# Kernel optimization log

Hardware: AMD Instinct MI355X
Metric: run time of the kernel (lower is better)

Reference implementation:

```python
import jax, jax.numpy as jnp
import numpy as np

SEQ, D, H = 4096, 1024, 1024


def setup_inputs() -> dict:
    key = jax.random.key(0)
    k_x, k_w1, k_b1, k_w2, k_b2 = jax.random.split(key, 5)
    std = 1.0 / np.sqrt(H)
    inputs = jax.random.normal(k_x, (SEQ, D), dtype=jnp.float32)
    W1 = jax.random.uniform(k_w1, (3 * H, 2 * D), minval=-std, maxval=std, dtype=jnp.float32)
    b1 = jax.random.uniform(k_b1, (3 * H,), minval=-std, maxval=std, dtype=jnp.float32)
    W2 = jax.random.uniform(k_w2, (H, H), minval=-std, maxval=std, dtype=jnp.float32)
    b2 = jax.random.uniform(k_b2, (H,), minval=-std, maxval=std, dtype=jnp.float32)
    return {"inputs": inputs, "W1": W1, "b1": b1, "W2": W2, "b2": b2}


def reference(inputs, W1, b1, W2, b2):
    # Exclusive prefix sum along seq: s[t] = sum_{i<t} x[i]
    s = jnp.concatenate(
        [jnp.zeros((1, inputs.shape[1]), dtype=inputs.dtype),
         jnp.cumsum(inputs[:-1], axis=0)], axis=0)
    v = jnp.concatenate([inputs, s], axis=1)            # [S, 2D]
    gates = v @ W1.T + b1                               # [S, 3H]
    ig, fg, h = jnp.split(gates, 3, axis=1)
    ig = jax.nn.sigmoid(ig)
    fg = jax.nn.sigmoid(fg)
    h = jnp.tanh(h) @ W2.T + b2                         # [S, H]
    hr = h * ig
    return (fg, hr)
```

## Files before the change

kernel.cpp:

```cpp
#include <hip/hip_runtime.h>
#include <cmath>

#define S_SEQ 4096
#define HD 1024
#define NG 3072
#define CHR 32
#define NCH 128
#define NZ 4

typedef _Float16 half8_t __attribute__((ext_vector_type(8)));
typedef _Float16 half4_t __attribute__((ext_vector_type(4)));
typedef float f32x4_t __attribute__((ext_vector_type(4)));

__device__ __forceinline__ void gload_lds16(const void* g, void* l) {
  __builtin_amdgcn_global_load_lds(
      (const __attribute__((address_space(1))) void*)g,
      (__attribute__((address_space(3))) void*)l, 16, 0, 0);
}

__device__ __forceinline__ float sigmoidf_(float x) {
  return 1.f / (1.f + __expf(-x));
}
__device__ __forceinline__ float tanhf_(float x) {
  return 1.f - 2.f / (__expf(2.f * x) + 1.f);
}

#define SCAN_BLOCKS 128
#define CONV_BLOCKS 7168
__global__ void prep(const float* __restrict__ W1, const float* __restrict__ W2,
                     _Float16* __restrict__ w1h, _Float16* __restrict__ w2h,
                     const float* __restrict__ x, _Float16* __restrict__ A,
                     _Float16* __restrict__ xsum) {
  const int bid = blockIdx.x;
  if (bid < SCAN_BLOCKS) {
    const int c = bid;
    const int j = threadIdx.x * 4;
    const int t0 = c * CHR;
    float4 run = make_float4(0.f, 0.f, 0.f, 0.f);
    for (int t = t0; t < t0 + CHR; t += 8) {
      float4 v[8];
#pragma unroll
      for (int u = 0; u < 8; ++u)
        v[u] = *(const float4*)&x[(size_t)(t + u) * HD + j];
#pragma unroll
      for (int u = 0; u < 8; ++u) {
        half4_t hx, hs;
        hx[0] = (_Float16)v[u].x;  hx[1] = (_Float16)v[u].y;
        hx[2] = (_Float16)v[u].z;  hx[3] = (_Float16)v[u].w;
        hs[0] = (_Float16)run.x;   hs[1] = (_Float16)run.y;
        hs[2] = (_Float16)run.z;   hs[3] = (_Float16)run.w;
        *(half4_t*)&A[(size_t)(t + u) * 2048 + j] = hx;
        *(half4_t*)&A[(size_t)(t + u) * 2048 + 1024 + j] = hs;
        run.x += v[u].x; run.y += v[u].y; run.z += v[u].z; run.w += v[u].w;
      }
    }
    half4_t hxs;
    hxs[0] = (_Float16)run.x; hxs[1] = (_Float16)run.y;
    hxs[2] = (_Float16)run.z; hxs[3] = (_Float16)run.w;
    *(half4_t*)&xsum[(size_t)c * HD + j] = hxs;
  } else {
    const int n1 = NG * 2048 / 4;
    int i = (bid - SCAN_BLOCKS) * 256 + threadIdx.x;
    const float* src = (i < n1) ? (W1 + (size_t)i * 4)
                                : (W2 + (size_t)(i - n1) * 4);
    _Float16* dst = (i < n1) ? (w1h + (size_t)i * 4)
                             : (w2h + (size_t)(i - n1) * 4);
    float4 v = *(const float4*)src;
    half4_t h;
    h[0] = (_Float16)v.x; h[1] = (_Float16)v.y;
    h[2] = (_Float16)v.z; h[3] = (_Float16)v.w;
    *(half4_t*)dst = h;
  }
}

__global__ void scan_part(const float* __restrict__ praw,
                          const float* __restrict__ b1,
                          float* __restrict__ pout) {
  int j = blockIdx.x * 256 + threadIdx.x;
  const size_t SP = (size_t)NCH * NG;
  float run = b1[j];
  for (int c = 0; c < NCH; c += 8) {
    float v[8];
#pragma unroll
    for (int u = 0; u < 8; ++u) {
      size_t i0 = (size_t)(c + u) * NG + j;
      v[u] = (praw[i0] + praw[i0 + SP]) + (praw[i0 + 2 * SP] + praw[i0 + 3 * SP]);
    }
#pragma unroll
    for (int u = 0; u < 8; ++u) {
      pout[(size_t)(c + u) * NG + j] = run;
      run += v[u];
    }
  }
}

__global__ __launch_bounds__(256, 2)
void gemm_part(const _Float16* __restrict__ A, const _Float16* __restrict__ B,
               float* __restrict__ C) {
  __shared__ _Float16 As[128 * 32];
  __shared__ _Float16 Bs[128 * 32];

  const int tid = threadIdx.x;
  const int lane = tid & 63;
  const int wid = tid >> 6;
  const int wr = wid >> 1;
  const int wc = wid & 1;

  const int n0 = blockIdx.x * 128;
  const int koff = blockIdx.z * (1024 / NZ);

  const int srow = lane >> 2;
  const int scol = (lane & 3) << 3;

  const _Float16* gA = A + (size_t)(wid * 32 + srow) * 1024 + koff + scol;
  const _Float16* gB = B + (size_t)(n0 + wid * 32 + srow) * 2048 + koff + scol;
  _Float16* lA = As + (wid * 32) * 32;
  _Float16* lB = Bs + (wid * 32) * 32;

  f32x4_t acc[4][4] = {};

  const int fr = lane & 15;
  const int fk = (lane >> 4) << 3;

  for (int kk = 0; kk < 1024 / NZ; kk += 32) {
    gload_lds16(gA + kk,                    lA);
    gload_lds16(gA + kk + (size_t)16*1024,  lA + 16 * 32);
    gload_lds16(gB + kk,                    lB);
    gload_lds16(gB + kk + (size_t)16*2048,  lB + 16 * 32);
    __syncthreads();

    half8_t af[4], bf[4];
#pragma unroll
    for (int m = 0; m < 4; ++m)
      af[m] = *(const half8_t*)&As[(wr * 64 + m * 16 + fr) * 32 + fk];
#pragma unroll
    for (int n = 0; n < 4; ++n)
      bf[n] = *(const half8_t*)&Bs[(wc * 64 + n * 16 + fr) * 32 + fk];
#pragma unroll
    for (int m = 0; m < 4; ++m)
#pragma unroll
      for (int n = 0; n < 4; ++n)
        acc[m][n] = __builtin_amdgcn_mfma_f32_16x16x32_f16(af[m], bf[n],
                                                           acc[m][n], 0, 0, 0);
    __syncthreads();
  }

  float* Cz = C + (size_t)blockIdx.z * NCH * NG;
  const int crow = wr * 64 + ((lane >> 4) << 2);
  const int ccol = n0 + wc * 64 + fr;
#pragma unroll
  for (int m = 0; m < 4; ++m)
#pragma unroll
    for (int n = 0; n < 4; ++n) {
      const int col = ccol + n * 16;
#pragma unroll
      for (int r = 0; r < 4; ++r)
        Cz[(size_t)(crow + m * 16 + r) * NG + col] = acc[m][n][r];
    }
}

#define BARX __builtin_amdgcn_s_barrier()
#define PR1 __builtin_amdgcn_s_setprio(1)
#define PR0 __builtin_amdgcn_s_setprio(0)

__global__ __launch_bounds__(256, 2)
void gemm1_k64(const _Float16* __restrict__ A, const _Float16* __restrict__ B,
               const float* __restrict__ part, _Float16* __restrict__ igb,
               float* __restrict__ out0, _Float16* __restrict__ th) {
  constexpr int KS = 2048;
  constexpr int NT = 32;
  __shared__ __align__(16) _Float16 sA[2][128 * 64];
  __shared__ __align__(16) _Float16 sB[2][192 * 64];

  const int tid = threadIdx.x;
  const int l = tid & 63;
  const int wid = tid >> 6;
  const int wr = wid >> 1;
  const int wc = wid & 1;

  const int bid = blockIdx.x;
  const int xcd = bid & 7;
  const int q = bid >> 3;
  const int by = xcd * 4 + q / 16;
  const int bx = q % 16;
  const int m0 = by * 128;
  const int n0 = bx * 192;

  const int rB = tid >> 3;
  const int cB = tid & 7;
  const int csw = (cB ^ (rB & 7)) << 3;
  const _Float16* gA0 = A + (size_t)(m0 + rB) * KS + csw;
  const _Float16* gB0 = B + (size_t)(n0 + rB) * KS + csw;
  const int dsto = rB * 64 + cB * 8;

#define STG(bb, kt) do {                                               \
    const int kk_ = (kt) * 64;                                         \
    _Pragma("unroll")                                                  \
    for (int j = 0; j < 4; ++j)                                        \
      gload_lds16(gA0 + (size_t)(32 * j) * KS + kk_,                   \
                  (_Float16*)&sA[bb][dsto + j * 2048]);                \
    _Pragma("unroll")                                                  \
    for (int j = 0; j < 6; ++j)                                        \
      gload_lds16(gB0 + (size_t)(32 * j) * KS + kk_,                   \
                  (_Float16*)&sB[bb][dsto + j * 2048]);                \
  } while (0)

  const int fr = l & 15;
  const int kq = l >> 4;

#define RDA(dst, M, H, bb) do {                                        \
    const int row_ = wr * 64 + (M) * 16 + fr;                          \
    dst = *(const half8_t*)&sA[bb][row_ * 64 +                         \
          ((((H) * 4 + kq) ^ (row_ & 7)) << 3)];                       \
  } while (0)
#define RDB(dst, N_, H, bb) do {                                       \
    const int row_ = wc * 96 + (N_) * 16 + fr;                         \
    dst = *(const half8_t*)&sB[bb][row_ * 64 +                         \
          ((((H) * 4 + kq) ^ (row_ & 7)) << 3)];                       \
  } while (0)

  f32x4_t acc[4][6] = {};

#define BODY(t, bb) do {                                               \
    const int nt_ = ((t) + 1 < NT) ? (t) + 1 : NT - 1;                 \
    STG((bb) ^ 1, nt_);                                                \
    half8_t af[4][2], bf[6][2];                                        \
    _Pragma("unroll")                                                  \
    for (int m = 0; m < 4; ++m) {                                      \
      RDA(af[m][0], m, 0, bb); RDA(af[m][1], m, 1, bb);                \
    }                                                                  \
    _Pragma("unroll")                                                  \
    for (int n = 0; n < 6; ++n) {                                      \
      RDB(bf[n][0], n, 0, bb); RDB(bf[n][1], n, 1, bb);                \
    }                                                                  \
    PR1;                                                               \
    _Pragma("unroll")                                                  \
    for (int m = 0; m < 4; ++m)                                        \
      _Pragma("unroll")                                                \
      for (int n = 0; n < 6; ++n) {                                    \
        acc[m][n] = __builtin_amdgcn_mfma_f32_16x16x32_f16(            \
            af[m][0], bf[n][0], acc[m][n], 0, 0, 0);                   \
        acc[m][n] = __builtin_amdgcn_mfma_f32_16x16x32_f16(            \
            af[m][1], bf[n][1], acc[m][n], 0, 0, 0);                   \
      }                                                                \
    PR0;                                                               \
    asm volatile("s_waitcnt vmcnt(0)" ::: "memory");                   \
    BARX;                                                              \
  } while (0)

  STG(0, 0);
  asm volatile("s_waitcnt vmcnt(0)" ::: "memory");
  BARX;

#pragma unroll 1
  for (int t2 = 0; t2 < NT / 2; ++t2) {
    BODY(2 * t2,     0);
    BODY(2 * t2 + 1, 1);
  }

  const int crow = m0 + wr * 64 + ((l >> 4) << 2);
  const int ccol = n0 + wc * 96 + fr;

  float pv[2][6];
  const int cbase = crow >> 5;
#pragma unroll
  for (int h = 0; h < 2; ++h)
#pragma unroll
    for (int n = 0; n < 6; ++n)
      pv[h][n] = part[(size_t)(cbase + h) * NG + ccol + n * 16];

#pragma unroll
  for (int m = 0; m < 4; ++m)
#pragma unroll
    for (int n = 0; n < 6; ++n) {
      const int col = ccol + n * 16;
#pragma unroll
      for (int r = 0; r < 4; ++r) {
        const int row = crow + m * 16 + r;
        float g = acc[m][n][r] + pv[m >> 1][n];
        if (col < 1024)
          igb[(size_t)row * HD + col] = (_Float16)sigmoidf_(g);
        else if (col < 2048)
          out0[(size_t)row * HD + (col - 1024)] = sigmoidf_(g);
        else
          th[(size_t)row * HD + (col - 2048)] = (_Float16)tanhf_(g);
      }
    }
#undef STG
#undef RDA
#undef RDB
#undef BODY
}

__global__ __launch_bounds__(256, 2)
void gemm2_k64(const _Float16* __restrict__ A, const _Float16* __restrict__ B,
               float* __restrict__ outf,
               const float* __restrict__ bias, const _Float16* __restrict__ mulh) {
  constexpr int KS = 1024;
  constexpr int NT = 16;
  __shared__ __align__(16) _Float16 sA[2][128 * 64];
  __shared__ __align__(16) _Float16 sB[2][64 * 64];

  const int tid = threadIdx.x;
  const int l = tid & 63;
  const int wid = tid >> 6;
  const int wr = wid >> 1;
  const int wc = wid & 1;

  const int bid = blockIdx.x;
  const int xcd = bid & 7;
  const int q = bid >> 3;
  const int by = xcd * 4 + q / 16;
  const int bx = q % 16;
  const int m0 = by * 128;
  const int n0 = bx * 64;

  const int rB = tid >> 3;
  const int cB = tid & 7;
  const int csw = (cB ^ (rB & 7)) << 3;
  const _Float16* gA0 = A + (size_t)(m0 + rB) * KS + csw;
  const _Float16* gB0 = B + (size_t)(n0 + rB) * KS + csw;
  const int dsto = rB * 64 + cB * 8;

#define STG(bb, kt) do {                                               \
    const int kk_ = (kt) * 64;                                         \
    _Pragma("unroll")                                                  \
    for (int j = 0; j < 4; ++j)                                        \
      gload_lds16(gA0 + (size_t)(32 * j) * KS + kk_,                   \
                  (_Float16*)&sA[bb][dsto + j * 2048]);                \
    _Pragma("unroll")                                                  \
    for (int j = 0; j < 2; ++j)                                        \
      gload_lds16(gB0 + (size_t)(32 * j) * KS + kk_,                   \
                  (_Float16*)&sB[bb][dsto + j * 2048]);                \
  } while (0)

  const int fr = l & 15;
  const int kq = l >> 4;

#define RDA(dst, M, H, bb) do {                                        \
    const int row_ = wr * 64 + (M) * 16 + fr;                          \
    dst = *(const half8_t*)&sA[bb][row_ * 64 +                         \
          ((((H) * 4 + kq) ^ (row_ & 7)) << 3)];                       \
  } while (0)
#define RDB(dst, N_, H, bb) do {                                       \
    const int row_ = wc * 32 + (N_) * 16 + fr;                         \
    dst = *(const half8_t*)&sB[bb][row_ * 64 +                         \
          ((((H) * 4 + kq) ^ (row_ & 7)) << 3)];                       \
  } while (0)

  f32x4_t acc[4][2] = {};

#define BODY(t, bb) do {                                               \
    const int nt_ = ((t) + 1 < NT) ? (t) + 1 : NT - 1;                 \
    STG((bb) ^ 1, nt_);                                                \
    half8_t af[4][2], bf[2][2];                                        \
    _Pragma("unroll")                                                  \
    for (int m = 0; m < 4; ++m) {                                      \
      RDA(af[m][0], m, 0, bb); RDA(af[m][1], m, 1, bb);                \
    }                                                                  \
    _Pragma("unroll")                                                  \
    for (int n = 0; n < 2; ++n) {                                      \
      RDB(bf[n][0], n, 0, bb); RDB(bf[n][1], n, 1, bb);                \
    }                                                                  \
    PR1;                                                               \
    _Pragma("unroll")                                                  \
    for (int m = 0; m < 4; ++m)                                        \
      _Pragma("unroll")                                                \
      for (int n = 0; n < 2; ++n) {                                    \
        acc[m][n] = __builtin_amdgcn_mfma_f32_16x16x32_f16(            \
            af[m][0], bf[n][0], acc[m][n], 0, 0, 0);                   \
        acc[m][n] = __builtin_amdgcn_mfma_f32_16x16x32_f16(            \
            af[m][1], bf[n][1], acc[m][n], 0, 0, 0);                   \
      }                                                                \
    PR0;                                                               \
    asm volatile("s_waitcnt vmcnt(0)" ::: "memory");                   \
    BARX;                                                              \
  } while (0)

  STG(0, 0);
  asm volatile("s_waitcnt vmcnt(0)" ::: "memory");
  BARX;

#pragma unroll 1
  for (int t2 = 0; t2 < NT / 2; ++t2) {
    BODY(2 * t2,     0);
    BODY(2 * t2 + 1, 1);
  }

  const int crow = m0 + wr * 64 + ((l >> 4) << 2);
  const int ccol = n0 + wc * 32 + fr;
#pragma unroll
  for (int m = 0; m < 4; ++m)
#pragma unroll
    for (int n = 0; n < 2; ++n) {
      const int col = ccol + n * 16;
#pragma unroll
      for (int r = 0; r < 4; ++r) {
        const int row = crow + m * 16 + r;
        size_t idx = (size_t)row * HD + col;
        outf[idx] = (acc[m][n][r] + bias[col]) * (float)mulh[idx];
      }
    }
#undef STG
#undef RDA
#undef RDB
#undef BODY
}

extern "C" void kernel_launch(void* const* d_in, const int* in_sizes, int n_in,
                              void* d_out, int out_size, void* d_ws, size_t ws_size,
                              hipStream_t stream) {
  const float* x  = (const float*)d_in[0];
  const float* W1 = (const float*)d_in[1];
  const float* b1 = (const float*)d_in[2];
  const float* W2 = (const float*)d_in[3];
  const float* b2 = (const float*)d_in[4];
  float* out0 = (float*)d_out;
  float* out1 = out0 + (size_t)S_SEQ * HD;

  char* ws = (char*)d_ws;
  _Float16* Ah    = (_Float16*)(ws);
  _Float16* w1h   = (_Float16*)(ws + ((size_t)16 << 20));
  _Float16* w2h   = (_Float16*)(ws + ((size_t)28 << 20));
  _Float16* xsumh = (_Float16*)(ws + ((size_t)30 << 20));
  float*    praw  = (float*)   (ws + ((size_t)31 << 20));
  float*    pout  = (float*)   (ws + ((size_t)37 << 20));
  _Float16* igb   = (_Float16*)(ws + ((size_t)39 << 20));
  _Float16* th    = (_Float16*)(ws + ((size_t)47 << 20));

  prep<<<dim3(SCAN_BLOCKS + CONV_BLOCKS), dim3(256), 0, stream>>>(
      W1, W2, w1h, w2h, x, Ah, xsumh);

  gemm_part<<<dim3(NG / 128, 1, NZ), dim3(256), 0, stream>>>(
      xsumh, w1h + 1024, praw);

  scan_part<<<dim3(NG / 256), dim3(256), 0, stream>>>(praw, b1, pout);

  gemm1_k64<<<dim3(512), dim3(256), 0, stream>>>(
      Ah, w1h, pout, igb, out0, th);

  gemm2_k64<<<dim3(512), dim3(256), 0, stream>>>(
      th, w2h, out1, b2, igb);
}
```

Baseline: 123.4 us.

## Rewrite chunk-sum partial GEMM with K64 swizzled double-buffered tiles and split-K 8

The small partial-sum GEMM that feeds the chunk scan is rebuilt on the same 128x192, K=64, XOR-swizzled, double-buffered LDS pipeline used by the main GEMMs. Split-K rises from 4 to 8 so the 16 N-tiles still fill the GPU, and scan_part now reduces 8 partial slices instead of 4. The main GEMM loops also skip the redundant prefetch on their last iteration. In exchange, the partial buffer doubles, so the workspace layout shifts and the scan reads more memory.

New measurement: 125.9 us. 1.02x slower.

```diff
diff --git a/kernel.cpp b/kernel.cpp
--- a/kernel.cpp
+++ b/kernel.cpp
@@ -6,7 +6,7 @@
 #define NG 3072
 #define CHR 32
 #define NCH 128
-#define NZ 4
+#define NZ 8
 
 typedef _Float16 half8_t __attribute__((ext_vector_type(8)));
 typedef _Float16 half4_t __attribute__((ext_vector_type(4)));
@@ -84,7 +84,11 @@
 #pragma unroll
     for (int u = 0; u < 8; ++u) {
       size_t i0 = (size_t)(c + u) * NG + j;
-      v[u] = (praw[i0] + praw[i0 + SP]) + (praw[i0 + 2 * SP] + praw[i0 + 3 * SP]);
+      float s0 = praw[i0]          + praw[i0 + SP];
+      float s1 = praw[i0 + 2 * SP] + praw[i0 + 3 * SP];
+      float s2 = praw[i0 + 4 * SP] + praw[i0 + 5 * SP];
+      float s3 = praw[i0 + 6 * SP] + praw[i0 + 7 * SP];
+      v[u] = (s0 + s1) + (s2 + s3);
     }
 #pragma unroll
     for (int u = 0; u < 8; ++u) {
@@ -94,74 +98,112 @@
   }
 }
 
+#define BARX __builtin_amdgcn_s_barrier()
+#define PR1 __builtin_amdgcn_s_setprio(1)
+#define PR0 __builtin_amdgcn_s_setprio(0)
+
 __global__ __launch_bounds__(256, 2)
-void gemm_part(const _Float16* __restrict__ A, const _Float16* __restrict__ B,
-               float* __restrict__ C) {
-  __shared__ _Float16 As[128 * 32];
-  __shared__ _Float16 Bs[128 * 32];
+void gemm_part_k64(const _Float16* __restrict__ A, const _Float16* __restrict__ B,
+                   float* __restrict__ C) {
+  constexpr int KSA = 1024, KSB = 2048;
+  constexpr int NT = 2;
+  __shared__ __align__(16) _Float16 sA[2][128 * 64];
+  __shared__ __align__(16) _Float16 sB[2][192 * 64];
 
   const int tid = threadIdx.x;
-  const int lane = tid & 63;
+  const int l = tid & 63;
   const int wid = tid >> 6;
   const int wr = wid >> 1;
   const int wc = wid & 1;
 
-  const int n0 = blockIdx.x * 128;
-  const int koff = blockIdx.z * (1024 / NZ);
-
-  const int srow = lane >> 2;
-  const int scol = (lane & 3) << 3;
-
-  const _Float16* gA = A + (size_t)(wid * 32 + srow) * 1024 + koff + scol;
-  const _Float16* gB = B + (size_t)(n0 + wid * 32 + srow) * 2048 + koff + scol;
-  _Float16* lA = As + (wid * 32) * 32;
-  _Float16* lB = Bs + (wid * 32) * 32;
-
-  f32x4_t acc[4][4] = {};
-
-  const int fr = lane & 15;
-  const int fk = (lane >> 4) << 3;
-
-  for (int kk = 0; kk < 1024 / NZ; kk += 32) {
-    gload_lds16(gA + kk,                    lA);
-    gload_lds16(gA + kk + (size_t)16*1024,  lA + 16 * 32);
-    gload_lds16(gB + kk,                    lB);
-    gload_lds16(gB + kk + (size_t)16*2048,  lB + 16 * 32);
-    __syncthreads();
-
-    half8_t af[4], bf[4];
-#pragma unroll
-    for (int m = 0; m < 4; ++m)
-      af[m] = *(const half8_t*)&As[(wr * 64 + m * 16 + fr) * 32 + fk];
-#pragma unroll
-    for (int n = 0; n < 4; ++n)
-      bf[n] = *(const half8_t*)&Bs[(wc * 64 + n * 16 + fr) * 32 + fk];
-#pragma unroll
-    for (int m = 0; m < 4; ++m)
-#pragma unroll
-      for (int n = 0; n < 4; ++n)
-        acc[m][n] = __builtin_amdgcn_mfma_f32_16x16x32_f16(af[m], bf[n],
-                                                           acc[m][n], 0, 0, 0);
-    __syncthreads();
-  }
+  const int n0 = blockIdx.x * 192;
+  const int koff = blockIdx.z * 128;
+
+  const int rB = tid >> 3;
+  const int cB = tid & 7;
+  const int csw = (cB ^ (rB & 7)) << 3;
+  const _Float16* gA0 = A + (size_t)rB * KSA + koff + csw;
+  const _Float16* gB0 = B + (size_t)(n0 + rB) * KSB + koff + csw;
+  const int dsto = rB * 64 + cB * 8;
+
+#define STG(bb, kt) do {                                               \
+    const int kk_ = (kt) * 64;                                         \
+    _Pragma("unroll")                                                  \
+    for (int j = 0; j < 4; ++j)                                        \
+      gload_lds16(gA0 + (size_t)(32 * j) * KSA + kk_,                  \
+                  (_Float16*)&sA[bb][dsto + j * 2048]);                \
+    _Pragma("unroll")                                                  \
+    for (int j = 0; j < 6; ++j)                                        \
+      gload_lds16(gB0 + (size_t)(32 * j) * KSB + kk_,                  \
+                  (_Float16*)&sB[bb][dsto + j * 2048]);                \
+  } while (0)
+
+  const int fr = l & 15;
+  const int kq = l >> 4;
+
+#define RDA(dst, M, H, bb) do {                                        \
+    const int row_ = wr * 64 + (M) * 16 + fr;                          \
+    dst = *(const half8_t*)&sA[bb][row_ * 64 +                         \
+          ((((H) * 4 + kq) ^ (row_ & 7)) << 3)];                       \
+  } while (0)
+#define RDB(dst, N_, H, bb) do {                                       \
+    const int row_ = wc * 96 + (N_) * 16 + fr;                         \
+    dst = *(const half8_t*)&sB[bb][row_ * 64 +                         \
+          ((((H) * 4 + kq) ^ (row_ & 7)) << 3)];                       \
+  } while (0)
+
+  f32x4_t acc[4][6] = {};
+
+#define BODY(t, bb) do {                                               \
+    if ((t) + 1 < NT) STG((bb) ^ 1, (t) + 1);                          \
+    half8_t af[4][2], bf[6][2];                                        \
+    _Pragma("unroll")                                                  \
+    for (int m = 0; m < 4; ++m) {                                      \
+      RDA(af[m][0], m, 0, bb); RDA(af[m][1], m, 1, bb);                \
+    }                                                                  \
+    _Pragma("unroll")                                                  \
+    for (int n = 0; n < 6; ++n) {                                      \
+      RDB(bf[n][0], n, 0, bb); RDB(bf[n][1], n, 1, bb);                \
+    }                                                                  \
+    PR1;                                                               \
+    _Pragma("unroll")                                                  \
+    for (int m = 0; m < 4; ++m)                                        \
+      _Pragma("unroll")                                                \
+      for (int n = 0; n < 6; ++n) {                                    \
+        acc[m][n] = __builtin_amdgcn_mfma_f32_16x16x32_f16(            \
+            af[m][0], bf[n][0], acc[m][n], 0, 0, 0);                   \
+        acc[m][n] = __builtin_amdgcn_mfma_f32_16x16x32_f16(            \
+            af[m][1], bf[n][1], acc[m][n], 0, 0, 0);                   \
+      }                                                                \
+    PR0;                                                               \
+    asm volatile("s_waitcnt vmcnt(0)" ::: "memory");                   \
+    BARX;                                                              \
+  } while (0)
+
+  STG(0, 0);
+  asm volatile("s_waitcnt vmcnt(0)" ::: "memory");
+  BARX;
+
+  BODY(0, 0);
+  BODY(1, 1);
 
   float* Cz = C + (size_t)blockIdx.z * NCH * NG;
-  const int crow = wr * 64 + ((lane >> 4) << 2);
-  const int ccol = n0 + wc * 64 + fr;
+  const int crow = wr * 64 + ((l >> 4) << 2);
+  const int ccol = n0 + wc * 96 + fr;
 #pragma unroll
   for (int m = 0; m < 4; ++m)
 #pragma unroll
-    for (int n = 0; n < 4; ++n) {
+    for (int n = 0; n < 6; ++n) {
       const int col = ccol + n * 16;
 #pragma unroll
       for (int r = 0; r < 4; ++r)
         Cz[(size_t)(crow + m * 16 + r) * NG + col] = acc[m][n][r];
     }
-}
-
-#define BARX __builtin_amdgcn_s_barrier()
-#define PR1 __builtin_amdgcn_s_setprio(1)
-#define PR0 __builtin_amdgcn_s_setprio(0)
+#undef STG
+#undef RDA
+#undef RDB
+#undef BODY
+}
 
 __global__ __launch_bounds__(256, 2)
 void gemm1_k64(const _Float16* __restrict__ A, const _Float16* __restrict__ B,
@@ -222,8 +264,7 @@
   f32x4_t acc[4][6] = {};
 
 #define BODY(t, bb) do {                                               \
-    const int nt_ = ((t) + 1 < NT) ? (t) + 1 : NT - 1;                 \
-    STG((bb) ^ 1, nt_);                                                \
+    if ((t) + 1 < NT) STG((bb) ^ 1, (t) + 1);                          \
     half8_t af[4][2], bf[6][2];                                        \
     _Pragma("unroll")                                                  \
     for (int m = 0; m < 4; ++m) {                                      \
@@ -351,8 +392,7 @@
   f32x4_t acc[4][2] = {};
 
 #define BODY(t, bb) do {                                               \
-    const int nt_ = ((t) + 1 < NT) ? (t) + 1 : NT - 1;                 \
-    STG((bb) ^ 1, nt_);                                                \
+    if ((t) + 1 < NT) STG((bb) ^ 1, (t) + 1);                          \
     half8_t af[4][2], bf[2][2];                                        \
     _Pragma("unroll")                                                  \
     for (int m = 0; m < 4; ++m) {                                      \
@@ -424,14 +464,14 @@
   _Float16* w2h   = (_Float16*)(ws + ((size_t)28 << 20));
   _Float16* xsumh = (_Float16*)(ws + ((size_t)30 << 20));
   float*    praw  = (float*)   (ws + ((size_t)31 << 20));
-  float*    pout  = (float*)   (ws + ((size_t)37 << 20));
-  _Float16* igb   = (_Float16*)(ws + ((size_t)39 << 20));
-  _Float16* th    = (_Float16*)(ws + ((size_t)47 << 20));
+  float*    pout  = (float*)   (ws + ((size_t)43 << 20));
+  _Float16* igb   = (_Float16*)(ws + ((size_t)45 << 20));
+  _Float16* th    = (_Float16*)(ws + ((size_t)53 << 20));
 
   prep<<<dim3(SCAN_BLOCKS + CONV_BLOCKS), dim3(256), 0, stream>>>(
       W1, W2, w1h, w2h, x, Ah, xsumh);
 
-  gemm_part<<<dim3(NG / 128, 1, NZ), dim3(256), 0, stream>>>(
+  gemm_part_k64<<<dim3(NG / 192, 1, NZ), dim3(256), 0, stream>>>(
       xsumh, w1h + 1024, praw);
 
   scan_part<<<dim3(NG / 256), dim3(256), 0, stream>>>(praw, b1, pout);
```
